# Kernel optimization log

Hardware: AMD Instinct MI355X
Metric: run time of the kernel (lower is better)

Reference implementation:

```python
import jax, jax.numpy as jnp
import numpy as np

DIM = 1024
HEADS = 16
HEAD_DIM = DIM // HEADS
B, N = 2, 2048
SCALE = 1.0 / np.float32(np.sqrt(DIM))  # original scales by sqrt(dim), not sqrt(head_dim)


def setup_inputs() -> dict:
    key = jax.random.key(0)
    ks = jax.random.split(key, 9)
    s = 0.02
    return {
        "x": jax.random.normal(ks[0], (B, N, DIM), dtype=jnp.float32),
        "Wq": jax.random.normal(ks[1], (DIM, DIM), dtype=jnp.float32) * s,
        "bq": jax.random.normal(ks[2], (DIM,), dtype=jnp.float32) * s,
        "Wk": jax.random.normal(ks[3], (DIM, DIM), dtype=jnp.float32) * s,
        "bk": jax.random.normal(ks[4], (DIM,), dtype=jnp.float32) * s,
        "Wv": jax.random.normal(ks[5], (DIM, DIM), dtype=jnp.float32) * s,
        "bv": jax.random.normal(ks[6], (DIM,), dtype=jnp.float32) * s,
        "Wo": jax.random.normal(ks[7], (DIM, DIM), dtype=jnp.float32) * s,
        "bo": jax.random.normal(ks[8], (DIM,), dtype=jnp.float32) * s,
    }


def _split_heads(t):
    # torch.stack(torch.split(t, head_dim, -1), dim=0) -> (H, B, N, head_dim)
    b, n, _ = t.shape
    return jnp.moveaxis(t.reshape(b, n, HEADS, HEAD_DIM), 2, 0)


def reference(x, Wq, bq, Wk, bk, Wv, bv, Wo, bo):
    q = _split_heads(x @ Wq.T + bq)  # (H,B,N,d)
    k = _split_heads(x @ Wk.T + bk)
    v = _split_heads(x @ Wv.T + bv)
    # NOTE: original computes K @ Q^T (K rows attend over Q rows), scaled by sqrt(dim)
    scores = jnp.einsum("hbnd,hbmd->hbnm", k, q) * SCALE  # (H,B,N,N)
    attn = jax.nn.softmax(scores, axis=-1)
    out = jnp.einsum("hbnm,hbmd->hbnd", attn, v)  # (H,B,N,d)
    out = jnp.moveaxis(out, 0, 2).reshape(x.shape[0], x.shape[1], DIM)  # (B,N,H*d)
    return out @ Wo.T + bo
```

## Files before the change

### kernel.cpp

```cpp
#include <hip/hip_runtime.h>
#include <hip/hip_bf16.h>
#include <cstdint>
#include <cstddef>

typedef __bf16 bf16_t;
typedef __bf16 bf16x4 __attribute__((ext_vector_type(4)));
typedef __bf16 bf16x8 __attribute__((ext_vector_type(8)));
typedef float  f32x4  __attribute__((ext_vector_type(4)));
typedef float  f32x16 __attribute__((ext_vector_type(16)));
typedef unsigned int u32;
typedef unsigned int u32x4 __attribute__((ext_vector_type(4)));

#define DIM_   1024
#define HEADS_ 16
#define HD_    64
#define BB_    2
#define NN_    2048
#define MTOT   (BB_*NN_)
static constexpr float SCALE_ = 0.03125f;
static constexpr float EXPC_  = 0.045084220027780106f;

__device__ __forceinline__ float exp2_hw(float x) {
    float r;
    asm("v_exp_f32 %0, %1" : "=v"(r) : "v"(x));
    return r;
}

__global__ __launch_bounds__(256) void cvt_all(
    const float* __restrict__ X,
    const float* __restrict__ W0, const float* __restrict__ W1,
    const float* __restrict__ W2, const float* __restrict__ W3,
    bf16_t* __restrict__ xo,
    bf16_t* __restrict__ o0, bf16_t* __restrict__ o1,
    bf16_t* __restrict__ o2, bf16_t* __restrict__ o3)
{
    const int bid = blockIdx.x;
    const float* src;
    bf16_t* dst;
    int lb;
    if (bid < 2048) { src = X; dst = xo; lb = bid; }
    else {
        const int w = (bid - 2048) >> 9;
        lb = (bid - 2048) & 511;
        src = (w == 0) ? W0 : (w == 1) ? W1 : (w == 2) ? W2 : W3;
        dst = (w == 0) ? o0 : (w == 1) ? o1 : (w == 2) ? o2 : o3;
    }
    const size_t i = ((size_t)lb * 256 + threadIdx.x) * 8;
    f32x4 a = *(const f32x4*)(src + i);
    f32x4 b = *(const f32x4*)(src + i + 4);
    bf16x8 o;
    o[0] = (bf16_t)a.x; o[1] = (bf16_t)a.y; o[2] = (bf16_t)a.z; o[3] = (bf16_t)a.w;
    o[4] = (bf16_t)b.x; o[5] = (bf16_t)b.y; o[6] = (bf16_t)b.z; o[7] = (bf16_t)b.w;
    *(bf16x8*)(dst + i) = o;
}

__device__ __forceinline__ void gld16(const bf16_t* g, bf16_t* l) {
    __builtin_amdgcn_global_load_lds(
        (const __attribute__((address_space(1))) unsigned int*)g,
        (__attribute__((address_space(3))) unsigned int*)l, 16, 0, 0);
}

__global__ __launch_bounds__(512) void gemm_qkv(
    const bf16_t* __restrict__ A,
    const bf16_t* __restrict__ Wq, const bf16_t* __restrict__ Wk, const bf16_t* __restrict__ Wv,
    const float* __restrict__ bq, const float* __restrict__ bk, const float* __restrict__ bv,
    bf16_t* __restrict__ Cq, bf16_t* __restrict__ Ck, bf16_t* __restrict__ Cv)
{
    __shared__ __align__(16) bf16_t As[2][128 * 32];
    __shared__ __align__(16) bf16_t Bs[2][3 * 64 * 32];

    const int tid  = threadIdx.x;
    const int lane = tid & 63;
    const int w    = tid >> 6;
    const int wr   = w >> 1;
    const int wc   = w & 1;
    const int bn   = blockIdx.x;
    const int bm   = blockIdx.y;

    const int l15 = lane & 15;
    const int g   = lane >> 4;

    const int srow = lane >> 2;
    const int scol = (lane & 3) * 8;

    const bf16_t* aSrc  = A + (size_t)(bm * 128 + 16 * w + srow) * DIM_ + scol;
    const bf16_t* w1p   = (w < 4) ? Wq : Wk;
    const bf16_t* b1Src = w1p + (size_t)(bn * 64 + 16 * (w & 3) + srow) * DIM_ + scol;
    const bf16_t* b2Src = Wv  + (size_t)(bn * 64 + 16 * w + srow) * DIM_ + scol;
    const int b1Off = ((w < 4) ? 0 : 2048) + (w & 3) * 512;
    const int b2Off = 4096 + w * 512;

    f32x4 aq[2][2], ak[2][2], av[2][2];
    #pragma unroll
    for (int i = 0; i < 2; i++)
        #pragma unroll
        for (int j = 0; j < 2; j++) {
            aq[i][j] = (f32x4){0.f, 0.f, 0.f, 0.f};
            ak[i][j] = (f32x4){0.f, 0.f, 0.f, 0.f};
            av[i][j] = (f32x4){0.f, 0.f, 0.f, 0.f};
        }

    #define QSTAGE(buf, kb)                                        \
        {                                                          \
            gld16(aSrc + (kb), &As[buf][w * 512]);                 \
            gld16(b1Src + (kb), &Bs[buf][b1Off]);                  \
            if (w < 4) gld16(b2Src + (kb), &Bs[buf][b2Off]);       \
        }

    QSTAGE(0, 0);
    __syncthreads();

    for (int t = 0; t < 32; t++) {
        const int cur = t & 1;
        if (t < 31) QSTAGE(cur ^ 1, (t + 1) * 32);

        bf16x8 af[2];
        #pragma unroll
        for (int i = 0; i < 2; i++)
            af[i] = *(const bf16x8*)&As[cur][(wr * 32 + i * 16 + l15) * 32 + g * 8];
        bf16x8 bqf[2], bkf[2], bvf[2];
        #pragma unroll
        for (int j = 0; j < 2; j++) {
            const int off = (wc * 32 + j * 16 + l15) * 32 + g * 8;
            bqf[j] = *(const bf16x8*)&Bs[cur][off];
            bkf[j] = *(const bf16x8*)&Bs[cur][2048 + off];
            bvf[j] = *(const bf16x8*)&Bs[cur][4096 + off];
        }
        #pragma unroll
        for (int i = 0; i < 2; i++)
            #pragma unroll
            for (int j = 0; j < 2; j++) {
                aq[i][j] = __builtin_amdgcn_mfma_f32_16x16x32_bf16(af[i], bqf[j], aq[i][j], 0, 0, 0);
                ak[i][j] = __builtin_amdgcn_mfma_f32_16x16x32_bf16(af[i], bkf[j], ak[i][j], 0, 0, 0);
                av[i][j] = __builtin_amdgcn_mfma_f32_16x16x32_bf16(af[i], bvf[j], av[i][j], 0, 0, 0);
            }

        __syncthreads();
    }
    #undef QSTAGE

    const int r4 = g * 4;
    #pragma unroll
    for (int j = 0; j < 2; j++) {
        const int gc = bn * 64 + wc * 32 + j * 16 + l15;
        const float vq = bq[gc], vk = bk[gc], vv = bv[gc];
        #pragma unroll
        for (int i = 0; i < 2; i++) {
            #pragma unroll
            for (int r = 0; r < 4; r++) {
                const size_t gr = (size_t)(bm * 128 + wr * 32 + i * 16 + r4 + r) * DIM_ + gc;
                Cq[gr] = (bf16_t)((aq[i][j][r] + vq) * EXPC_);
                Ck[gr] = (bf16_t)(ak[i][j][r] + vk);
                Cv[gr] = (bf16_t)(av[i][j][r] + vv);
            }
        }
    }
}

__global__ __launch_bounds__(512) void gemm_o(
    const bf16_t* __restrict__ A, const bf16_t* __restrict__ Wo,
    const float* __restrict__ bo, float* __restrict__ C)
{
    __shared__ __align__(16) bf16_t As[2][64 * 64];
    __shared__ __align__(16) bf16_t Bs[2][128 * 64];

    const int tid  = threadIdx.x;
    const int lane = tid & 63;
    const int w    = tid >> 6;
    const int wr   = w & 1;
    const int wc   = w >> 1;
    const int bn   = blockIdx.x;
    const int bm   = blockIdx.y;

    const int l15 = lane & 15;
    const int g   = lane >> 4;

    const int srow = lane >> 3;
    const int scol = (lane & 7) * 8;

    const bf16_t* aSrc  = A  + (size_t)(bm * 64 + w * 8 + srow) * DIM_ + scol;
    const bf16_t* b0Src = Wo + (size_t)(bn * 128 + (w * 2 + 0) * 8 + srow) * DIM_ + scol;
    const bf16_t* b1Src = Wo + (size_t)(bn * 128 + (w * 2 + 1) * 8 + srow) * DIM_ + scol;

    f32x4 acc[2][2];
    #pragma unroll
    for (int i = 0; i < 2; i++)
        #pragma unroll
        for (int j = 0; j < 2; j++)
            acc[i][j] = (f32x4){0.f, 0.f, 0.f, 0.f};

    #define OSTAGE(buf, kb)                                          \
        {                                                            \
            gld16(aSrc + (kb), &As[buf][w * 512]);                   \
            gld16(b0Src + (kb), &Bs[buf][(w * 2 + 0) * 512]);        \
            gld16(b1Src + (kb), &Bs[buf][(w * 2 + 1) * 512]);        \
        }

    OSTAGE(0, 0);
    __syncthreads();

    for (int t = 0; t < 16; t++) {
        const int cur = t & 1;
        if (t < 15) OSTAGE(cur ^ 1, (t + 1) * 64);

        #pragma unroll
        for (int kk = 0; kk < 2; kk++) {
            bf16x8 af[2], bf[2];
            #pragma unroll
            for (int i = 0; i < 2; i++)
                af[i] = *(const bf16x8*)&As[cur][(wr * 32 + i * 16 + l15) * 64 + kk * 32 + g * 8];
            #pragma unroll
            for (int j = 0; j < 2; j++)
                bf[j] = *(const bf16x8*)&Bs[cur][(wc * 32 + j * 16 + l15) * 64 + kk * 32 + g * 8];
            #pragma unroll
            for (int i = 0; i < 2; i++)
                #pragma unroll
                for (int j = 0; j < 2; j++)
                    acc[i][j] = __builtin_amdgcn_mfma_f32_16x16x32_bf16(af[i], bf[j], acc[i][j], 0, 0, 0);
        }

        __syncthreads();
    }
    #undef OSTAGE

    const int r4 = g * 4;
    #pragma unroll
    for (int j = 0; j < 2; j++) {
        const int gc = bn * 128 + wc * 32 + j * 16 + l15;
        const float bv = bo[gc];
        #pragma unroll
        for (int i = 0; i < 2; i++) {
            #pragma unroll
            for (int r = 0; r < 4; r++) {
                const size_t gr = (size_t)(bm * 64 + wr * 32 + i * 16 + r4 + r) * DIM_ + gc;
                C[gr] = acc[i][j][r] + bv;
            }
        }
    }
}

__global__ __launch_bounds__(256) void transpose_v(
    const bf16_t* __restrict__ V, bf16_t* __restrict__ Vt)
{
    __shared__ __align__(16) bf16_t Ts[64 * 72];
    const int tid = threadIdx.x;
    const int mt  = blockIdx.x;
    const int bh  = blockIdx.y;
    const int b   = bh >> 4, h = bh & 15;
    const int m0  = mt * 64;
    const int r   = tid >> 2;
    const int c   = (tid & 3) * 16;

    const bf16x8* s = (const bf16x8*)(V + ((size_t)(b * NN_ + m0 + r)) * DIM_ + h * HD_ + c);
    *(bf16x8*)(Ts + r * 72 + c)     = s[0];
    *(bf16x8*)(Ts + r * 72 + c + 8) = s[1];
    __syncthreads();

    bf16x8 o0, o1;
    #pragma unroll
    for (int i = 0; i < 8; i++) o0[i] = Ts[(c + i) * 72 + r];
    #pragma unroll
    for (int i = 0; i < 8; i++) o1[i] = Ts[(c + 8 + i) * 72 + r];
    bf16_t* dst = Vt + ((size_t)bh * HD_ + r) * NN_ + m0 + c;
    *(bf16x8*)dst       = o0;
    *(bf16x8*)(dst + 8) = o1;
}

__device__ __forceinline__ u32 cvtpk_bf16(float lo, float hi) {
    u32 d;
    asm volatile("v_cvt_pk_bf16_f32 %0, %1, %2" : "=v"(d) : "v"(lo), "v"(hi));
    return d;
}

__global__ __launch_bounds__(512, 4) void attn_mfma9(
    const bf16_t* __restrict__ Qa,
    const bf16_t* __restrict__ Ka,
    const bf16_t* __restrict__ Vtg,
    bf16_t* __restrict__ O)
{
    __shared__ __align__(16) bf16_t Kt[2][128 * 72];
    __shared__ __align__(16) bf16_t Vt[2][64 * 136];

    const int tid  = threadIdx.x;
    const int lane = tid & 63;
    const int w    = tid >> 6;
    const int l31  = lane & 31;
    const int h5   = lane >> 5;

    const int nw = (w & 3) * 32;
    const int mo = (w >> 2) * 64;

    const int wg = blockIdx.x;
    const int id = (wg & 7) * 64 + (wg >> 3);
    const int bh = id >> 4;
    const int nt = id & 15;
    const int b  = bh >> 4, h = bh & 15;
    const int n0 = nt * 128;

    const size_t base = (size_t)b * NN_ * DIM_ + h * HD_;

    const bf16_t* qrow = Qa + base + (size_t)(n0 + nw + l31) * DIM_ + h5 * 8;
    bf16x8 qf[4];
    #pragma unroll
    for (int ks = 0; ks < 4; ks++)
        qf[ks] = *(const bf16x8*)(qrow + ks * 16);

    f32x16 oa0 = {}, oa1 = {};
    float Lp = 0.f;

    const bf16_t* vrow   = Vtg + (size_t)bh * HD_ * NN_;
    const bf16_t* kgbase = Ka + base;

    const int kr2 = tid >> 3;
    const int kc2 = (tid & 7) * 8;
    const int vc2 = (tid & 7) * 16;

    bf16x8 kA0, kB0, vA0, vA1;

    #define ISSUE(m0)                                                                        \
        {                                                                                    \
            kA0 = *(const bf16x8*)(kgbase + (size_t)((m0) + kr2) * DIM_ + kc2);              \
            kB0 = *(const bf16x8*)(kgbase + (size_t)((m0) + 64 + kr2) * DIM_ + kc2);         \
            const bf16x8* vp = (const bf16x8*)(vrow + (size_t)kr2 * NN_ + (m0) + vc2);       \
            vA0 = vp[0]; vA1 = vp[1];                                                        \
        }
    #define COMMIT(buf)                                                                      \
        {                                                                                    \
            *(bf16x8*)(Kt[buf] + kr2 * 72 + kc2)        = kA0;                               \
            *(bf16x8*)(Kt[buf] + (64 + kr2) * 72 + kc2) = kB0;                               \
            bf16_t* vd = Vt[buf] + kr2 * 136 + vc2;                                          \
            *(bf16x8*)(vd)     = vA0;                                                        \
            *(bf16x8*)(vd + 8) = vA1;                                                        \
        }

    ISSUE(0);
    COMMIT(0);
    __syncthreads();

    for (int mt = 0; mt < NN_ / 128; mt++) {
        const int cur = mt & 1;
        if (mt < NN_ / 128 - 1) ISSUE((mt + 1) * 128);

        const bf16_t* KtC = Kt[cur];
        const bf16_t* VtC = Vt[cur];

        f32x16 sa0 = {}, sa1 = {};
        __builtin_amdgcn_s_setprio(1);
        #pragma unroll
        for (int ks = 0; ks < 4; ks++) {
            bf16x8 kf0 = *(const bf16x8*)&KtC[(mo + l31) * 72 + ks * 16 + h5 * 8];
            bf16x8 kf1 = *(const bf16x8*)&KtC[(mo + 32 + l31) * 72 + ks * 16 + h5 * 8];
            sa0 = __builtin_amdgcn_mfma_f32_32x32x16_bf16(kf0, qf[ks], sa0, 0, 0, 0);
            sa1 = __builtin_amdgcn_mfma_f32_32x32x16_bf16(kf1, qf[ks], sa1, 0, 0, 0);
        }
        __builtin_amdgcn_s_setprio(0);

        float p0[16], p1[16];
        #pragma unroll
        for (int r = 0; r < 16; r++) { p0[r] = exp2_hw(sa0[r]); p1[r] = exp2_hw(sa1[r]); }
        {
            float s0 = (p0[0] + p0[1]) + (p0[2] + p0[3]);
            float s1 = (p0[4] + p0[5]) + (p0[6] + p0[7]);
            float s2 = (p0[8] + p0[9]) + (p0[10] + p0[11]);
            float s3 = (p0[12] + p0[13]) + (p0[14] + p0[15]);
            float t0 = (p1[0] + p1[1]) + (p1[2] + p1[3]);
            float t1 = (p1[4] + p1[5]) + (p1[6] + p1[7]);
            float t2 = (p1[8] + p1[9]) + (p1[10] + p1[11]);
            float t3 = (p1[12] + p1[13]) + (p1[14] + p1[15]);
            Lp += ((s0 + s1) + (s2 + s3)) + ((t0 + t1) + (t2 + t3));
        }

        bf16x8 pf[4];
        #pragma unroll
        for (int mb = 0; mb < 4; mb++) {
            const float* pp = (mb & 2) ? p1 : p0;
            const int rb = (mb & 1) * 8;
            u32 x0 = cvtpk_bf16(pp[rb + 0], pp[rb + 1]);
            u32 x1 = cvtpk_bf16(pp[rb + 2], pp[rb + 3]);
            u32 y0 = cvtpk_bf16(pp[rb + 4], pp[rb + 5]);
            u32 y1 = cvtpk_bf16(pp[rb + 6], pp[rb + 7]);
            asm volatile("v_permlane32_swap_b32 %0, %1" : "+v"(x0), "+v"(y0));
            asm volatile("v_permlane32_swap_b32 %0, %1" : "+v"(x1), "+v"(y1));
            u32x4 t; t.x = x0; t.y = x1; t.z = y0; t.w = y1;
            pf[mb] = __builtin_bit_cast(bf16x8, t);
        }

        __builtin_amdgcn_s_setprio(1);
        #pragma unroll
        for (int ms = 0; ms < 4; ms++) {
            bf16x8 vf0 = *(const bf16x8*)&VtC[l31 * 136 + mo + ms * 16 + h5 * 8];
            bf16x8 vf1 = *(const bf16x8*)&VtC[(32 + l31) * 136 + mo + ms * 16 + h5 * 8];
            oa0 = __builtin_amdgcn_mfma_f32_32x32x16_bf16(pf[ms], vf0, oa0, 0, 0, 0);
            oa1 = __builtin_amdgcn_mfma_f32_32x32x16_bf16(pf[ms], vf1, oa1, 0, 0, 0);
        }
        __builtin_amdgcn_s_setprio(0);

        if (mt < NN_ / 128 - 1) COMMIT(cur ^ 1);
        __syncthreads();
    }
    #undef ISSUE
    #undef COMMIT

    Lp += __shfl_xor(Lp, 32);

    float* scratch0 = (float*)Kt;
    float* scratch1 = (float*)Vt;
    if (w >= 4) {
        float* buf = (w < 6) ? (scratch0 + (w - 4) * 2112)
                             : (scratch1 + (w - 6) * 2112);
        #pragma unroll
        for (int reg = 0; reg < 16; reg++) {
            buf[reg * 64 + lane]        = oa0[reg];
            buf[1024 + reg * 64 + lane] = oa1[reg];
        }
        buf[2048 + lane] = Lp;
    }
    __syncthreads();
    if (w < 4) {
        const float* buf = (w < 2) ? (scratch0 + w * 2112)
                                   : (scratch1 + (w - 2) * 2112);
        #pragma unroll
        for (int reg = 0; reg < 16; reg++) {
            oa0[reg] += buf[reg * 64 + lane];
            oa1[reg] += buf[1024 + reg * 64 + lane];
        }
        Lp += buf[2048 + lane];
    }
    __syncthreads();

    float* Lsh = scratch0 + 4224;
    if (w < 4) Lsh[nw + l31] = Lp;
    __syncthreads();

    if (w < 4) {
        #pragma unroll
        for (int reg = 0; reg < 16; reg++) {
            const int nr = (reg & 3) + 8 * (reg >> 2) + 4 * h5;
            const float il = 1.f / Lsh[nw + nr];
            const size_t rowoff = base + (size_t)(n0 + nw + nr) * DIM_;
            O[rowoff + l31]      = (bf16_t)(oa0[reg] * il);
            O[rowoff + 32 + l31] = (bf16_t)(oa1[reg] * il);
        }
    }
}

extern "C" void kernel_launch(void* const* d_in, const int* in_sizes, int n_in,
                              void* d_out, int out_size, void* d_ws, size_t ws_size,
                              hipStream_t stream)
{
    const float* x  = (const float*)d_in[0];
    const float* Wq = (const float*)d_in[1];
    const float* bq = (const float*)d_in[2];
    const float* Wk = (const float*)d_in[3];
    const float* bk = (const float*)d_in[4];
    const float* Wv = (const float*)d_in[5];
    const float* bv = (const float*)d_in[6];
    const float* Wo = (const float*)d_in[7];
    const float* bo = (const float*)d_in[8];
    float* out = (float*)d_out;

    const size_t SEG = (size_t)MTOT * DIM_;
    bf16_t* xb = (bf16_t*)d_ws;
    bf16_t* qb = xb + SEG;
    bf16_t* kb = qb + SEG;
    bf16_t* vb = kb + SEG;
    bf16_t* vt = xb;
    bf16_t* ab = vb;

    bf16_t* wqb = vb + SEG;
    bf16_t* wkb = wqb + (size_t)DIM_ * DIM_;
    bf16_t* wvb = wkb + (size_t)DIM_ * DIM_;
    bf16_t* wob = wvb + (size_t)DIM_ * DIM_;

    cvt_all<<<dim3(4096), 256, 0, stream>>>(x, Wq, Wk, Wv, Wo, xb, wqb, wkb, wvb, wob);

    gemm_qkv<<<dim3(16, 32), 512, 0, stream>>>(
        xb, wqb, wkb, wvb, bq, bk, bv, qb, kb, vb);

    dim3 gt(NN_ / 64, BB_ * HEADS_);
    transpose_v<<<gt, 256, 0, stream>>>(vb, vt);

    attn_mfma9<<<dim3(512), 512, 0, stream>>>(kb, qb, vt, ab);

    gemm_o<<<dim3(8, 64), 512, 0, stream>>>(ab, wob, bo, out);
}
```

Baseline: 118.1 us.

## Fuse V transpose into QKV GEMM epilogue and widen K tile to 64

The QKV projection kernel now writes V directly in transposed per-head layout through a shared-memory staging tile, so the separate transpose_v kernel and its extra read and write of V are removed. The K-step of the GEMM is doubled from 32 to 64, which halves the number of loop iterations and barriers but doubles LDS use per block. The workspace aliasing is rearranged so the attention output reuses the x buffer. Risks are lower occupancy from the larger LDS footprint and bank conflicts in the transposed LDS scatter.

```diff
diff --git a/kernel.cpp b/kernel.cpp
--- a/kernel.cpp
+++ b/kernel.cpp
@@ -64,10 +64,10 @@
     const bf16_t* __restrict__ A,
     const bf16_t* __restrict__ Wq, const bf16_t* __restrict__ Wk, const bf16_t* __restrict__ Wv,
     const float* __restrict__ bq, const float* __restrict__ bk, const float* __restrict__ bv,
-    bf16_t* __restrict__ Cq, bf16_t* __restrict__ Ck, bf16_t* __restrict__ Cv)
+    bf16_t* __restrict__ Cq, bf16_t* __restrict__ Ck, bf16_t* __restrict__ Vt)
 {
-    __shared__ __align__(16) bf16_t As[2][128 * 32];
-    __shared__ __align__(16) bf16_t Bs[2][3 * 64 * 32];
+    __shared__ __align__(16) bf16_t As[2][128 * 64];
+    __shared__ __align__(16) bf16_t Bs[2][3 * 64 * 64];
 
     const int tid  = threadIdx.x;
     const int lane = tid & 63;
@@ -80,15 +80,14 @@
     const int l15 = lane & 15;
     const int g   = lane >> 4;
 
-    const int srow = lane >> 2;
-    const int scol = (lane & 3) * 8;
-
-    const bf16_t* aSrc  = A + (size_t)(bm * 128 + 16 * w + srow) * DIM_ + scol;
-    const bf16_t* w1p   = (w < 4) ? Wq : Wk;
-    const bf16_t* b1Src = w1p + (size_t)(bn * 64 + 16 * (w & 3) + srow) * DIM_ + scol;
-    const bf16_t* b2Src = Wv  + (size_t)(bn * 64 + 16 * w + srow) * DIM_ + scol;
-    const int b1Off = ((w < 4) ? 0 : 2048) + (w & 3) * 512;
-    const int b2Off = 4096 + w * 512;
+    const int srow = lane >> 3;
+    const int scol = (lane & 7) * 8;
+
+    const bf16_t* aSrc0 = A  + (size_t)(bm * 128 + (w * 2 + 0) * 8 + srow) * DIM_ + scol;
+    const bf16_t* aSrc1 = A  + (size_t)(bm * 128 + (w * 2 + 1) * 8 + srow) * DIM_ + scol;
+    const bf16_t* qSrc  = Wq + (size_t)(bn * 64 + w * 8 + srow) * DIM_ + scol;
+    const bf16_t* kSrc  = Wk + (size_t)(bn * 64 + w * 8 + srow) * DIM_ + scol;
+    const bf16_t* vSrc  = Wv + (size_t)(bn * 64 + w * 8 + srow) * DIM_ + scol;
 
     f32x4 aq[2][2], ak[2][2], av[2][2];
     #pragma unroll
@@ -100,60 +99,80 @@
             av[i][j] = (f32x4){0.f, 0.f, 0.f, 0.f};
         }
 
-    #define QSTAGE(buf, kb)                                        \
-        {                                                          \
-            gld16(aSrc + (kb), &As[buf][w * 512]);                 \
-            gld16(b1Src + (kb), &Bs[buf][b1Off]);                  \
-            if (w < 4) gld16(b2Src + (kb), &Bs[buf][b2Off]);       \
+    #define QSTAGE(buf, kb)                                       \
+        {                                                         \
+            gld16(aSrc0 + (kb), &As[buf][(w * 2 + 0) * 512]);     \
+            gld16(aSrc1 + (kb), &As[buf][(w * 2 + 1) * 512]);     \
+            gld16(qSrc + (kb), &Bs[buf][w * 512]);                \
+            gld16(kSrc + (kb), &Bs[buf][4096 + w * 512]);         \
+            gld16(vSrc + (kb), &Bs[buf][8192 + w * 512]);         \
         }
 
     QSTAGE(0, 0);
     __syncthreads();
 
-    for (int t = 0; t < 32; t++) {
+    for (int t = 0; t < 16; t++) {
         const int cur = t & 1;
-        if (t < 31) QSTAGE(cur ^ 1, (t + 1) * 32);
-
-        bf16x8 af[2];
-        #pragma unroll
-        for (int i = 0; i < 2; i++)
-            af[i] = *(const bf16x8*)&As[cur][(wr * 32 + i * 16 + l15) * 32 + g * 8];
-        bf16x8 bqf[2], bkf[2], bvf[2];
-        #pragma unroll
-        for (int j = 0; j < 2; j++) {
-            const int off = (wc * 32 + j * 16 + l15) * 32 + g * 8;
-            bqf[j] = *(const bf16x8*)&Bs[cur][off];
-            bkf[j] = *(const bf16x8*)&Bs[cur][2048 + off];
-            bvf[j] = *(const bf16x8*)&Bs[cur][4096 + off];
-        }
-        #pragma unroll
-        for (int i = 0; i < 2; i++)
+        if (t < 15) QSTAGE(cur ^ 1, (t + 1) * 64);
+
+        #pragma unroll
+        for (int kk = 0; kk < 2; kk++) {
+            bf16x8 af[2];
+            #pragma unroll
+            for (int i = 0; i < 2; i++)
+                af[i] = *(const bf16x8*)&As[cur][(wr * 32 + i * 16 + l15) * 64 + kk * 32 + g * 8];
+            bf16x8 bqf[2], bkf[2], bvf[2];
             #pragma unroll
             for (int j = 0; j < 2; j++) {
-                aq[i][j] = __builtin_amdgcn_mfma_f32_16x16x32_bf16(af[i], bqf[j], aq[i][j], 0, 0, 0);
-                ak[i][j] = __builtin_amdgcn_mfma_f32_16x16x32_bf16(af[i], bkf[j], ak[i][j], 0, 0, 0);
-                av[i][j] = __builtin_amdgcn_mfma_f32_16x16x32_bf16(af[i], bvf[j], av[i][j], 0, 0, 0);
+                const int off = (wc * 32 + j * 16 + l15) * 64 + kk * 32 + g * 8;
+                bqf[j] = *(const bf16x8*)&Bs[cur][off];
+                bkf[j] = *(const bf16x8*)&Bs[cur][4096 + off];
+                bvf[j] = *(const bf16x8*)&Bs[cur][8192 + off];
             }
+            #pragma unroll
+            for (int i = 0; i < 2; i++)
+                #pragma unroll
+                for (int j = 0; j < 2; j++) {
+                    aq[i][j] = __builtin_amdgcn_mfma_f32_16x16x32_bf16(af[i], bqf[j], aq[i][j], 0, 0, 0);
+                    ak[i][j] = __builtin_amdgcn_mfma_f32_16x16x32_bf16(af[i], bkf[j], ak[i][j], 0, 0, 0);
+                    av[i][j] = __builtin_amdgcn_mfma_f32_16x16x32_bf16(af[i], bvf[j], av[i][j], 0, 0, 0);
+                }
+        }
 
         __syncthreads();
     }
     #undef QSTAGE
 
+    bf16_t* Ts = (bf16_t*)As;
     const int r4 = g * 4;
     #pragma unroll
     for (int j = 0; j < 2; j++) {
-        const int gc = bn * 64 + wc * 32 + j * 16 + l15;
+        const int lc = wc * 32 + j * 16 + l15;
+        const int gc = bn * 64 + lc;
         const float vq = bq[gc], vk = bk[gc], vv = bv[gc];
         #pragma unroll
         for (int i = 0; i < 2; i++) {
             #pragma unroll
             for (int r = 0; r < 4; r++) {
-                const size_t gr = (size_t)(bm * 128 + wr * 32 + i * 16 + r4 + r) * DIM_ + gc;
+                const int lm = wr * 32 + i * 16 + r4 + r;
+                const size_t gr = (size_t)(bm * 128 + lm) * DIM_ + gc;
                 Cq[gr] = (bf16_t)((aq[i][j][r] + vq) * EXPC_);
                 Ck[gr] = (bf16_t)(ak[i][j][r] + vk);
-                Cv[gr] = (bf16_t)(av[i][j][r] + vv);
+                Ts[lc * 136 + lm] = (bf16_t)(av[i][j][r] + vv);
             }
         }
+    }
+    __syncthreads();
+    {
+        const int b  = bm >> 4;
+        const int m0 = (bm & 15) * 128;
+        const int d  = tid >> 3;
+        const int c  = (tid & 7) * 16;
+        bf16x8 v0 = *(const bf16x8*)&Ts[d * 136 + c];
+        bf16x8 v1 = *(const bf16x8*)&Ts[d * 136 + c + 8];
+        bf16_t* dst = Vt + ((size_t)(b * HEADS_ + bn) * HD_ + d) * NN_ + m0 + c;
+        *(bf16x8*)dst       = v0;
+        *(bf16x8*)(dst + 8) = v1;
     }
 }
 
@@ -237,33 +256,6 @@
             }
         }
     }
-}
-
-__global__ __launch_bounds__(256) void transpose_v(
-    const bf16_t* __restrict__ V, bf16_t* __restrict__ Vt)
-{
-    __shared__ __align__(16) bf16_t Ts[64 * 72];
-    const int tid = threadIdx.x;
-    const int mt  = blockIdx.x;
-    const int bh  = blockIdx.y;
-    const int b   = bh >> 4, h = bh & 15;
-    const int m0  = mt * 64;
-    const int r   = tid >> 2;
-    const int c   = (tid & 3) * 16;
-
-    const bf16x8* s = (const bf16x8*)(V + ((size_t)(b * NN_ + m0 + r)) * DIM_ + h * HD_ + c);
-    *(bf16x8*)(Ts + r * 72 + c)     = s[0];
-    *(bf16x8*)(Ts + r * 72 + c + 8) = s[1];
-    __syncthreads();
-
-    bf16x8 o0, o1;
-    #pragma unroll
-    for (int i = 0; i < 8; i++) o0[i] = Ts[(c + i) * 72 + r];
-    #pragma unroll
-    for (int i = 0; i < 8; i++) o1[i] = Ts[(c + 8 + i) * 72 + r];
-    bf16_t* dst = Vt + ((size_t)bh * HD_ + r) * NN_ + m0 + c;
-    *(bf16x8*)dst       = o0;
-    *(bf16x8*)(dst + 8) = o1;
 }
 
 __device__ __forceinline__ u32 cvtpk_bf16(float lo, float hi) {
@@ -463,11 +455,10 @@
     bf16_t* xb = (bf16_t*)d_ws;
     bf16_t* qb = xb + SEG;
     bf16_t* kb = qb + SEG;
-    bf16_t* vb = kb + SEG;
-    bf16_t* vt = xb;
-    bf16_t* ab = vb;
-
-    bf16_t* wqb = vb + SEG;
+    bf16_t* vt = kb + SEG;
+    bf16_t* ab = xb;
+
+    bf16_t* wqb = vt + SEG;
     bf16_t* wkb = wqb + (size_t)DIM_ * DIM_;
     bf16_t* wvb = wkb + (size_t)DIM_ * DIM_;
     bf16_t* wob = wvb + (size_t)DIM_ * DIM_;
@@ -475,10 +466,7 @@
     cvt_all<<<dim3(4096), 256, 0, stream>>>(x, Wq, Wk, Wv, Wo, xb, wqb, wkb, wvb, wob);
 
     gemm_qkv<<<dim3(16, 32), 512, 0, stream>>>(
-        xb, wqb, wkb, wvb, bq, bk, bv, qb, kb, vb);
-
-    dim3 gt(NN_ / 64, BB_ * HEADS_);
-    transpose_v<<<gt, 256, 0, stream>>>(vb, vt);
+        xb, wqb, wkb, wvb, bq, bk, bv, qb, kb, vt);
 
     attn_mfma9<<<dim3(512), 512, 0, stream>>>(kb, qb, vt, ab);
 
```

Result: no change. 118.9 us (+0.7%).
